# Kernel optimization log

Measured on AMD Instinct MI355X. Metric: run time of the kernel, lower is better.

The kernel has to match this reference:

```python
import jax, jax.numpy as jnp
import numpy as np

DIM = 1024
D_STATE = 16
D_CONV = 4
EXPAND = 2
D_INNER = EXPAND * DIM          # 2048
DT_RANK = DIM // 16             # 64 (ceil(1024/16))
BATCH = 4096
LN_EPS = 1e-5


def setup_inputs() -> dict:
    key = jax.random.key(0)
    ks = jax.random.split(key, 8)
    s = lambda k, shape, sc=0.02: (jax.random.normal(k, shape, jnp.float32) * sc)
    return {
        "x": jax.random.normal(ks[0], (BATCH, DIM), jnp.float32),
        "ln_gamma": jnp.ones((DIM,), jnp.float32),
        "ln_beta": jnp.zeros((DIM,), jnp.float32),
        "W_in": s(ks[1], (2 * D_INNER, DIM)),            # in_proj (no bias)
        "conv_w": s(ks[2], (D_INNER, D_CONV), 0.2),      # depthwise causal conv
        "conv_b": jnp.zeros((D_INNER,), jnp.float32),
        "W_xproj": s(ks[3], (DT_RANK + 2 * D_STATE, D_INNER)),
        "W_dt": s(ks[4], (D_INNER, DT_RANK), 0.1),
        "b_dt": s(ks[5], (D_INNER,), 0.5),
        "A_log": jnp.log(jnp.broadcast_to(
            jnp.arange(1, D_STATE + 1, dtype=jnp.float32), (D_INNER, D_STATE))),
        "Dskip": jnp.ones((D_INNER,), jnp.float32),
        "W_out": s(ks[6], (DIM, D_INNER)),               # out_proj (no bias)
    }


def _mamba_layer(x, ln_gamma, ln_beta, W_in, conv_w, conv_b,
                 W_xproj, W_dt, b_dt, A_log, Dskip, W_out):
    # x: [B, dim] -> unsqueeze(1): [B, L=1, dim]
    xs = x[:, None, :]
    # LayerNorm over last dim
    mu = jnp.mean(xs, axis=-1, keepdims=True)
    var = jnp.var(xs, axis=-1, keepdims=True)
    xn = (xs - mu) * jax.lax.rsqrt(var + LN_EPS) * ln_gamma + ln_beta
    # in_proj -> split into x, z   [B, L, d_inner] each
    xz = jnp.einsum('bld,ed->ble', xn, W_in)
    xi, z = jnp.split(xz, 2, axis=-1)
    L = xi.shape[1]
    # depthwise causal conv1d (kernel d_conv, left pad d_conv-1)
    xp = jnp.pad(xi, ((0, 0), (D_CONV - 1, 0), (0, 0)))
    xc = conv_b + sum(conv_w[:, k] * xp[:, k:k + L, :] for k in range(D_CONV))
    xc = jax.nn.silu(xc)
    # x_proj -> dt, B, C
    xdb = jnp.einsum('bld,ed->ble', xc, W_xproj)
    dt, Bm, Cm = jnp.split(xdb, [DT_RANK, DT_RANK + D_STATE], axis=-1)
    dt = jax.nn.softplus(jnp.einsum('blr,dr->bld', dt, W_dt) + b_dt)  # [B,L,d_inner]
    A = -jnp.exp(A_log)                                              # [d_inner,d_state]
    dA = jnp.exp(dt[..., None] * A)                                  # [B,L,d_inner,d_state]
    dBu = dt[..., None] * Bm[:, :, None, :] * xc[..., None]          # [B,L,d_inner,d_state]

    def step(h, inp):
        dA_l, dBu_l, C_l = inp
        h = dA_l * h + dBu_l                    # [B,d_inner,d_state]
        y = jnp.einsum('bdn,bn->bd', h, C_l)    # [B,d_inner]
        return h, y

    h0 = jnp.zeros((x.shape[0], D_INNER, D_STATE), x.dtype)
    _, ys = jax.lax.scan(step, h0, (dA.swapaxes(0, 1), dBu.swapaxes(0, 1), Cm.swapaxes(0, 1)))
    y = ys.swapaxes(0, 1) + Dskip * xc          # [B,L,d_inner]
    y = y * jax.nn.silu(z)
    out = jnp.einsum('ble,de->bld', y, W_out)   # [B,L,dim]
    return out[:, 0, :]                          # squeeze(1)


def reference(x, ln_gamma, ln_beta, W_in, conv_w, conv_b,
              W_xproj, W_dt, b_dt, A_log, Dskip, W_out):
    return _mamba_layer(x, ln_gamma, ln_beta, W_in, conv_w, conv_b,
                        W_xproj, W_dt, b_dt, A_log, Dskip, W_out)
```

## Files before the change

### kernel.cpp

```cpp
#include <hip/hip_runtime.h>
#include <hip/hip_bf16.h>
#include <stdint.h>

#define DIM     1024
#define DINNER  2048
#define BATCH   4096
#define LN_EPS  1e-5f

typedef unsigned short u16;
using f32x4  = __attribute__((ext_vector_type(4))) float;
using bf16x8 = __attribute__((ext_vector_type(8))) __bf16;

__device__ __forceinline__ float bf2f(u16 h) {
    union { unsigned u; float f; } v; v.u = ((unsigned)h) << 16; return v.f;
}
__device__ __forceinline__ u16 f2bf(float f) {
    union { float f; unsigned u; } v; v.f = f;
    unsigned r = v.u + 0x7fffu + ((v.u >> 16) & 1u);
    return (u16)(r >> 16);
}
__device__ __forceinline__ float silu_f(float x) {
    return x / (1.f + __expf(-x));
}

#define AS1 __attribute__((address_space(1)))
#define AS3 __attribute__((address_space(3)))

__device__ __forceinline__ unsigned lds_u32(const void* p) {
    return (unsigned)(unsigned long long)(const AS3 void*)p;
}

__global__ __launch_bounds__(256)
void cvt_ln(const float* __restrict__ x, const float* __restrict__ gamma,
            const float* __restrict__ beta, u16* __restrict__ xn,
            const float4* __restrict__ s0, ushort4* __restrict__ d0, int n0,
            const float4* __restrict__ s1, ushort4* __restrict__ d1, int n1,
            const float4* __restrict__ s2, ushort4* __restrict__ d2, int n2,
            const float4* __restrict__ s3, ushort4* __restrict__ d3, int n3)
{
    const int t = threadIdx.x;
    if (blockIdx.x < BATCH) {
        const int row = blockIdx.x;
        float4 v = ((const float4*)(x + (size_t)row * DIM))[t];
        float s1v = v.x + v.y + v.z + v.w;
        float s2v = v.x*v.x + v.y*v.y + v.z*v.z + v.w*v.w;
        #pragma unroll
        for (int o = 32; o > 0; o >>= 1) {
            s1v += __shfl_down(s1v, o);
            s2v += __shfl_down(s2v, o);
        }
        __shared__ float red[8];
        __shared__ float mv[2];
        const int w = t >> 6, l = t & 63;
        if (l == 0) { red[w] = s1v; red[4 + w] = s2v; }
        __syncthreads();
        if (t == 0) {
            float a = red[0] + red[1] + red[2] + red[3];
            float b = red[4] + red[5] + red[6] + red[7];
            float mu = a * (1.f / DIM);
            float var = b * (1.f / DIM) - mu * mu;
            mv[0] = mu; mv[1] = rsqrtf(var + LN_EPS);
        }
        __syncthreads();
        const float mu = mv[0], rs = mv[1];
        float4 g  = ((const float4*)gamma)[t];
        float4 be = ((const float4*)beta)[t];
        ushort4 o = make_ushort4(
            f2bf((v.x - mu) * rs * g.x + be.x),
            f2bf((v.y - mu) * rs * g.y + be.y),
            f2bf((v.z - mu) * rs * g.z + be.z),
            f2bf((v.w - mu) * rs * g.w + be.w));
        *(ushort4*)(xn + (size_t)row * DIM + t * 4) = o;
    } else {
        int i = (blockIdx.x - BATCH) * 256 + t;
        const int stride = (gridDim.x - BATCH) * 256;
        const int total = n0 + n1 + n2 + n3;
        for (; i < total; i += stride) {
            int j = i; const float4* s; ushort4* d;
            if (j < n0) { s = s0; d = d0; }
            else { j -= n0;
                if (j < n1) { s = s1; d = d1; }
                else { j -= n1;
                    if (j < n2) { s = s2; d = d2; }
                    else { j -= n2; s = s3; d = d3; }
                }
            }
            float4 v = s[j];
            d[j] = make_ushort4(f2bf(v.x), f2bf(v.y), f2bf(v.z), f2bf(v.w));
        }
    }
}

#define DSR(d, adr, OFFSTR) \
    asm volatile("ds_read_b128 %0, %1 offset:" OFFSTR : "=v"(d) : "v"(adr))
#define RD_A8(DST, A0, A1, S0, S1, S2, S3) do { \
    DSR(DST[0][0], A0, S0); DSR(DST[0][1], A1, S0); \
    DSR(DST[1][0], A0, S1); DSR(DST[1][1], A1, S1); \
    DSR(DST[2][0], A0, S2); DSR(DST[2][1], A1, S2); \
    DSR(DST[3][0], A0, S3); DSR(DST[3][1], A1, S3); } while (0)
#define RD_B4(DST, A0, A1, S0, S1) do { \
    DSR(DST[0][0], A0, S0); DSR(DST[0][1], A1, S0); \
    DSR(DST[1][0], A0, S1); DSR(DST[1][1], A1, S1); } while (0)

#define BC8(x) __builtin_bit_cast(bf16x8, x)
#define MF1(C, Av, Bv) C = __builtin_amdgcn_mfma_f32_16x16x32_bf16(BC8(Av), BC8(Bv), C, 0, 0, 0)

#define CL32_LO do { \
    _Pragma("unroll") for (int m = 0; m < 4; ++m) \
    _Pragma("unroll") for (int n = 0; n < 2; ++n) \
    _Pragma("unroll") for (int k = 0; k < 2; ++k) { \
        MF1(acc[m][n],     aLo[m][k], bC0[n][k]); \
        MF1(acc[m][n + 2], aLo[m][k], bC1[n][k]); } } while (0)
#define CL16_HI0 do { \
    _Pragma("unroll") for (int m = 0; m < 4; ++m) \
    _Pragma("unroll") for (int n = 0; n < 2; ++n) \
    _Pragma("unroll") for (int k = 0; k < 2; ++k) \
        MF1(acc[4 + m][n], aHi[m][k], bC0[n][k]); } while (0)
#define CL16_HI1 do { \
    _Pragma("unroll") for (int m = 0; m < 4; ++m) \
    _Pragma("unroll") for (int n = 0; n < 2; ++n) \
    _Pragma("unroll") for (int k = 0; k < 2; ++k) \
        MF1(acc[4 + m][n + 2], aHi[m][k], bC1[n][k]); } while (0)

#define WAIT_LGKM8 do { asm volatile("s_waitcnt lgkmcnt(8)" ::: "memory"); \
    __builtin_amdgcn_sched_barrier(0); } while (0)
#define WAIT_LGKM0 do { asm volatile("s_waitcnt lgkmcnt(0)" ::: "memory"); \
    __builtin_amdgcn_sched_barrier(0); } while (0)

#define TILE_BODY(CA0, CA1, NA0, NA1, NB0, NB1, SDA0, SDA1, SDB0, SDB1, KT) do { \
    RD_A8(aHi, CA0, CA1, "8192", "10240", "12288", "14336"); \
    WAIT_LGKM8; \
    __builtin_amdgcn_s_setprio(1); CL32_LO; __builtin_amdgcn_s_setprio(0); \
    WAIT_LGKM0; \
    asm volatile("s_waitcnt vmcnt(0)" ::: "memory"); \
    __builtin_amdgcn_s_barrier(); \
    stage(SDB0, Bb, KT); stage(SDB1, BbH, KT); \
    stage(SDA0, Ab, KT); stage(SDA1, AbH, KT); \
    __builtin_amdgcn_s_setprio(1); CL16_HI0; __builtin_amdgcn_s_setprio(0); \
    RD_B4(bC0, NB0, NB1, "0", "2048"); \
    RD_A8(aLo, NA0, NA1, "0", "2048", "4096", "6144"); \
    __builtin_amdgcn_s_setprio(1); CL16_HI1; __builtin_amdgcn_s_setprio(0); \
    RD_B4(bC1, NB0, NB1, "4096", "6144"); \
} while (0)

__global__ __launch_bounds__(512, 2)
void gemmP(const u16* __restrict__ A, const u16* __restrict__ B,
           int N, int K, int nkt,
           u16* __restrict__ dst0, u16* __restrict__ dst1,
           const float* __restrict__ conv_w, const float* __restrict__ conv_b)
{
    __shared__ __align__(16) u16 lds[2][4][8192];
    const int tid = threadIdx.x;
    const int wid = tid >> 6, l = tid & 63;
    const int wm = wid >> 2, wn = wid & 3;
    const int lr = l & 15, l16 = l >> 4;

    const int lin = blockIdx.y * 16 + blockIdx.x;
    const int xcd = lin & 7, q = lin >> 3;
    const int by = (xcd & 3) * 4 + (q >> 3);
    const int bx = (xcd >> 2) * 8 + (q & 7);
    const int brow = by * 256, bcol = bx * 256;

    const int sr = tid >> 3;
    const int skk = ((tid & 7) ^ (sr & 7)) * 8;
    const u16* Ab  = A + (size_t)(brow + sr) * K + skk;
    const u16* Bb  = B + (size_t)(bcol + sr) * K + skk;
    const u16* AbH = Ab + (size_t)128 * K;
    const u16* BbH = Bb + (size_t)128 * K;

    u16* const dA0h0 = &lds[0][0][tid * 8]; u16* const dA0h1 = &lds[0][1][tid * 8];
    u16* const dA1h0 = &lds[1][0][tid * 8]; u16* const dA1h1 = &lds[1][1][tid * 8];
    u16* const dB0h0 = &lds[0][2][tid * 8]; u16* const dB0h1 = &lds[0][3][tid * 8];
    u16* const dB1h0 = &lds[1][2][tid * 8]; u16* const dB1h1 = &lds[1][3][tid * 8];

    const unsigned cxb0 = (unsigned)(((0 + l16) ^ (l & 7)) * 16);
    const unsigned cxb1 = (unsigned)(((4 + l16) ^ (l & 7)) * 16);
    const unsigned aB0 = lds_u32(&lds[0][wm][0]) + (unsigned)(lr * 128);
    const unsigned bB0 = lds_u32(&lds[0][2 + (wn >> 1)][0]) + (unsigned)((wn & 1) * 8192 + lr * 128);
    const unsigned adA00 = aB0 + cxb0, adA01 = aB0 + cxb1;
    const unsigned adA10 = adA00 + 65536, adA11 = adA01 + 65536;
    const unsigned adB00 = bB0 + cxb0, adB01 = bB0 + cxb1;
    const unsigned adB10 = adB00 + 65536, adB11 = adB01 + 65536;

    f32x4 acc[8][4] = {};
    float4 aLo[4][2], aHi[4][2], bC0[2][2], bC1[2][2];

    auto stage = [&](u16* dst, const u16* srcrow, int kt) {
        const u16* s = srcrow + (size_t)kt * 64;
        __builtin_amdgcn_global_load_lds((const AS1 void*)s, (AS3 void*)dst, 16, 0, 0);
        __builtin_amdgcn_global_load_lds((const AS1 void*)(s + (size_t)64 * K),
                                         (AS3 void*)(dst + 4096), 16, 0, 0);
    };

    stage(dB0h0, Bb, 0);  stage(dB0h1, BbH, 0);
    stage(dA0h0, Ab, 0);  stage(dA0h1, AbH, 0);
    stage(dB1h0, Bb, 1);  stage(dB1h1, BbH, 1);
    stage(dA1h0, Ab, 1);  stage(dA1h1, AbH, 1);
    asm volatile("s_waitcnt vmcnt(8)" ::: "memory");
    __builtin_amdgcn_s_barrier();
    RD_B4(bC0, adB00, adB01, "0", "2048");
    RD_B4(bC1, adB00, adB01, "4096", "6144");
    RD_A8(aLo, adA00, adA01, "0", "2048", "4096", "6144");

    const int niter = nkt >> 1;
    for (int i = 0; i < niter; ++i) {
        const int T = 2 * i;
        const int k2 = (T + 2 < nkt) ? T + 2 : nkt - 1;
        const int k3 = (T + 3 < nkt) ? T + 3 : nkt - 1;
        TILE_BODY(adA00, adA01, adA10, adA11, adB10, adB11,
                  dA0h0, dA0h1, dB0h0, dB0h1, k2);
        TILE_BODY(adA10, adA11, adA00, adA01, adB00, adB01,
                  dA1h0, dA1h1, dB1h0, dB1h1, k3);
    }

    asm volatile("s_waitcnt vmcnt(0) lgkmcnt(0)" ::: "memory");
    __builtin_amdgcn_s_barrier();

    float cb[4], cw[4];
    const bool isxc = (bcol < DINNER);
    if (isxc) {
        #pragma unroll
        for (int n = 0; n < 4; ++n) {
            const int cg = bcol + wn * 64 + n * 16 + lr;
            cb[n] = conv_b[cg]; cw[n] = conv_w[cg * 4 + 3];
        }
    }
    u16* eb = &lds[0][0][0];
    #pragma unroll
    for (int m = 0; m < 8; ++m)
        #pragma unroll
        for (int n = 0; n < 4; ++n)
            #pragma unroll
            for (int r = 0; r < 4; ++r) {
                const int rl = wm * 128 + m * 16 + l16 * 4 + r;
                const int cl = wn * 64 + n * 16 + lr;
                float v = acc[m][n][r];
                v = isxc ? silu_f(cb[n] + cw[n] * v) : silu_f(v);
                eb[rl * 256 + (cl ^ ((rl & 15) << 4))] = f2bf(v);
            }
    __syncthreads();

    u16* base = isxc ? (dst0 + bcol) : (dst1 + (bcol - DINNER));
    #pragma unroll
    for (int it = 0; it < 16; ++it) {
        const int idx = it * 4096 + tid * 8;
        const int r = idx >> 8, c = idx & 255;
        uint4 v = *(const uint4*)(eb + r * 256 + ((c ^ ((r & 15) << 4))));
        *(uint4*)(base + (size_t)(brow + r) * DINNER + c) = v;
    }
}

__global__ __launch_bounds__(256)
void gemm_xproj(const u16* __restrict__ xcb, const u16* __restrict__ Wx,
                float* __restrict__ P)
{
    __shared__ __align__(16) u16 Xs[64 * 64];
    __shared__ __align__(16) u16 Ws[96 * 64];
    const int t = threadIdx.x, w = t >> 6, l = t & 63;
    const int brow = blockIdx.x * 64;
    const int ks = blockIdx.y;
    const int lr = l & 15, l16 = l >> 4;
    const int skk = ((l & 7) ^ (l >> 3)) * 8;
    const u16* Xbase = xcb + (size_t)(brow + (l >> 3)) * DINNER + skk;
    const u16* Wbase = Wx + (size_t)(l >> 3) * DINNER + skk;

    f32x4 acc[6] = {};
    const int kend = ks * 512 + 512;
    for (int k0 = ks * 512; k0 < kend; k0 += 64) {
        #pragma unroll
        for (int c = 0; c < 2; ++c) {
            const int seg = c * 4 + w;
            __builtin_amdgcn_global_load_lds(
                (const AS1 void*)(Xbase + (size_t)seg * 8 * DINNER + k0),
                (AS3 void*)(&Xs[seg * 512]), 16, 0, 0);
        }
        #pragma unroll
        for (int c = 0; c < 3; ++c) {
            const int seg = c * 4 + w;
            __builtin_amdgcn_global_load_lds(
                (const AS1 void*)(Wbase + (size_t)seg * 8 * DINNER + k0),
                (AS3 void*)(&Ws[seg * 512]), 16, 0, 0);
        }
        __syncthreads();
        #pragma unroll
        for (int kk = 0; kk < 2; ++kk) {
            const int ra = w * 16 + lr;
            bf16x8 av = *(const bf16x8*)(&Xs[ra * 64 + (((kk * 4 + l16) ^ (ra & 7)) * 8)]);
            #pragma unroll
            for (int n = 0; n < 6; ++n) {
                const int rb = n * 16 + lr;
                bf16x8 bv = *(const bf16x8*)(&Ws[rb * 64 + (((kk * 4 + l16) ^ (rb & 7)) * 8)]);
                acc[n] = __builtin_amdgcn_mfma_f32_16x16x32_bf16(av, bv, acc[n], 0, 0, 0);
            }
        }
        __syncthreads();
    }
    #pragma unroll
    for (int n = 0; n < 6; ++n)
        #pragma unroll
        for (int r = 0; r < 4; ++r) {
            const int row = brow + w * 16 + l16 * 4 + r;
            const int col = n * 16 + lr;
            P[((size_t)ks * 96 + col) * BATCH + row] = acc[n][r];
        }
}

__global__ __launch_bounds__(256)
void finish_xdb(const float* __restrict__ P, u16* __restrict__ dtb, float* __restrict__ sbuf)
{
    const int b = blockIdx.x * 256 + threadIdx.x;
    #pragma unroll 8
    for (int c = 0; c < 64; ++c) {
        float v = P[((size_t)0 * 96 + c) * BATCH + b] + P[((size_t)1 * 96 + c) * BATCH + b]
                + P[((size_t)2 * 96 + c) * BATCH + b] + P[((size_t)3 * 96 + c) * BATCH + b];
        dtb[(size_t)b * 64 + c] = f2bf(v);
    }
    float s = 0.f;
    for (int n = 0; n < 16; ++n) {
        float Bv = 0.f, Cv = 0.f;
        #pragma unroll
        for (int ks = 0; ks < 4; ++ks) {
            Bv += P[((size_t)ks * 96 + 64 + n) * BATCH + b];
            Cv += P[((size_t)ks * 96 + 80 + n) * BATCH + b];
        }
        s += Bv * Cv;
    }
    sbuf[b] = s;
}

__global__ __launch_bounds__(256)
void gemm_dt_y(const u16* __restrict__ dtb, const u16* __restrict__ Wdt,
               const float* __restrict__ b_dt, const float* __restrict__ Dskip,
               const float* __restrict__ s,
               const u16* __restrict__ xcb, const u16* __restrict__ szb,
               u16* __restrict__ y)
{
    __shared__ __align__(16) u16 Ds[64 * 64];
    __shared__ __align__(16) u16 Ws[128 * 64];
    __shared__ __align__(16) u16 dts[64 * 128];
    const int t = threadIdx.x, w = t >> 6, l = t & 63;
    const int wr = w >> 1, wc = w & 1;
    const int brow = blockIdx.y * 64;
    const int bcol = blockIdx.x * 128;
    const int lr = l & 15, l16 = l >> 4;
    const int skk = ((l & 7) ^ (l >> 3)) * 8;

    {
        const u16* Dbase = dtb + (size_t)(brow + (l >> 3)) * 64 + skk;
        const u16* Wbase = Wdt + (size_t)(bcol + (l >> 3)) * 64 + skk;
        #pragma unroll
        for (int c = 0; c < 2; ++c) {
            const int seg = c * 4 + w;
            __builtin_amdgcn_global_load_lds(
                (const AS1 void*)(Dbase + (size_t)seg * 8 * 64),
                (AS3 void*)(&Ds[seg * 512]), 16, 0, 0);
        }
        #pragma unroll
        for (int c = 0; c < 4; ++c) {
            const int seg = c * 4 + w;
            __builtin_amdgcn_global_load_lds(
                (const AS1 void*)(Wbase + (size_t)seg * 8 * 64),
                (AS3 void*)(&Ws[seg * 512]), 16, 0, 0);
        }
    }
    __syncthreads();

    f32x4 acc[2][4] = {};
    #pragma unroll
    for (int kk = 0; kk < 2; ++kk) {
        bf16x8 av[2], bv[4];
        #pragma unroll
        for (int m = 0; m < 2; ++m) {
            const int r = wr * 32 + m * 16 + lr;
            av[m] = *(const bf16x8*)(&Ds[r * 64 + (((kk * 4 + l16) ^ (r & 7)) * 8)]);
        }
        #pragma unroll
        for (int n = 0; n < 4; ++n) {
            const int r = wc * 64 + n * 16 + lr;
            bv[n] = *(const bf16x8*)(&Ws[r * 64 + (((kk * 4 + l16) ^ (r & 7)) * 8)]);
        }
        #pragma unroll
        for (int m = 0; m < 2; ++m)
            #pragma unroll
            for (int n = 0; n < 4; ++n)
                acc[m][n] = __builtin_amdgcn_mfma_f32_16x16x32_bf16(av[m], bv[n], acc[m][n], 0, 0, 0);
    }

    #pragma unroll
    for (int m = 0; m < 2; ++m)
        #pragma unroll
        for (int n = 0; n < 4; ++n)
            #pragma unroll
            for (int r = 0; r < 4; ++r) {
                const int row = wr * 32 + m * 16 + l16 * 4 + r;
                const int col = wc * 64 + n * 16 + lr;
                float v = acc[m][n][r] + b_dt[bcol + col];
                float dt = (v > 20.f) ? v : log1pf(__expf(v));
                dts[row * 128 + (col ^ ((row & 7) << 4))] = f2bf(dt);
            }
    __syncthreads();

    const int rlo = t >> 4;
    const int cg  = (t & 15) * 8;
    #pragma unroll
    for (int rr = 0; rr < 4; ++rr) {
        const int row = rr * 16 + rlo;
        const int grow = brow + row;
        const float sr = s[grow];
        uint4 dv = *(const uint4*)(&dts[row * 128 + ((cg ^ ((row & 7) << 4)))]);
        uint4 xv = *(const uint4*)(xcb + (size_t)grow * DINNER + bcol + cg);
        uint4 zv = *(const uint4*)(szb + (size_t)grow * DINNER + bcol + cg);
        float4 D0 = *(const float4*)(Dskip + bcol + cg);
        float4 D1 = *(const float4*)(Dskip + bcol + cg + 4);
        const float* Dp = &D0.x;
        uint4 ov;
        unsigned* op = (unsigned*)&ov;
        #pragma unroll
        for (int k = 0; k < 4; ++k) {
            unsigned du = ((const unsigned*)&dv)[k];
            unsigned xu = ((const unsigned*)&xv)[k];
            unsigned zu = ((const unsigned*)&zv)[k];
            float Da = (k < 2) ? Dp[2 * k]     : (&D1.x)[2 * (k - 2)];
            float Db = (k < 2) ? Dp[2 * k + 1] : (&D1.x)[2 * (k - 2) + 1];
            float y0 = (bf2f((u16)du) * sr + Da) * bf2f((u16)xu) * bf2f((u16)zu);
            float y1 = (bf2f((u16)(du >> 16)) * sr + Db) * bf2f((u16)(xu >> 16)) * bf2f((u16)(zu >> 16));
            op[k] = (unsigned)f2bf(y0) | ((unsigned)f2bf(y1) << 16);
        }
        *(uint4*)(y + (size_t)grow * DINNER + bcol + cg) = ov;
    }
}

__global__ __launch_bounds__(256, 2)
void gemm4n(const u16* __restrict__ A, const u16* __restrict__ Bm,
            float* __restrict__ out)
{
    __shared__ __align__(16) u16 lds[2][12288];
    const int t = threadIdx.x, w = t >> 6, l = t & 63;
    const int wr = w >> 1, wc = w & 1;
    const int lr = l & 15, l16 = l >> 4;

    const int lin = blockIdx.y * 8 + blockIdx.x;
    const int xcd = lin & 7, q = lin >> 3;
    const int by = xcd * 8 + (q >> 3);
    const int bx = q & 7;
    const int brow = by * 64, bcol = bx * 128;
    const int K = DINNER, nkt = 32;

    auto stage = [&](int buf, int kt) {
        #pragma unroll
        for (int c = 0; c < 2; ++c) {
            const int o = c * 256 + t;
            const int sr = o >> 3;
            const int sc = (o & 7) ^ (sr & 7);
            __builtin_amdgcn_global_load_lds(
                (const AS1 void*)(A + (size_t)(brow + sr) * K + kt * 64 + sc * 8),
                (AS3 void*)(&lds[buf][o * 8]), 16, 0, 0);
        }
        #pragma unroll
        for (int c = 0; c < 4; ++c) {
            const int o = c * 256 + t;
            const int sr = o >> 3;
            const int sc = (o & 7) ^ (sr & 7);
            __builtin_amdgcn_global_load_lds(
                (const AS1 void*)(Bm + (size_t)(bcol + sr) * K + kt * 64 + sc * 8),
                (AS3 void*)(&lds[buf][4096 + o * 8]), 16, 0, 0);
        }
    };

    f32x4 acc[2][4] = {};

    stage(0, 0);
    stage(1, 1);
    asm volatile("s_waitcnt vmcnt(6)" ::: "memory");
    __builtin_amdgcn_s_barrier();

    for (int kt = 0; kt < nkt; ++kt) {
        const int cur = kt & 1;
        #pragma unroll
        for (int kk = 0; kk < 2; ++kk) {
            bf16x8 af[2], bf[4];
            #pragma unroll
            for (int m = 0; m < 2; ++m) {
                const int r = wr * 32 + m * 16 + lr;
                af[m] = *(const bf16x8*)(&lds[cur][r * 64 + (((kk * 4 + l16) ^ (r & 7)) * 8)]);
            }
            #pragma unroll
            for (int n = 0; n < 4; ++n) {
                const int r = wc * 64 + n * 16 + lr;
                bf[n] = *(const bf16x8*)(&lds[cur][4096 + r * 64 + (((kk * 4 + l16) ^ (r & 7)) * 8)]);
            }
            #pragma unroll
            for (int m = 0; m < 2; ++m)
                #pragma unroll
                for (int n = 0; n < 4; ++n)
                    acc[m][n] = __builtin_amdgcn_mfma_f32_16x16x32_bf16(af[m], bf[n], acc[m][n], 0, 0, 0);
        }
        __builtin_amdgcn_sched_barrier(0);
        __builtin_amdgcn_s_barrier();
        const int t2 = (kt + 2 < nkt) ? kt + 2 : nkt - 1;
        stage(cur, t2);
        asm volatile("s_waitcnt vmcnt(6)" ::: "memory");
        __builtin_amdgcn_sched_barrier(0);
        __builtin_amdgcn_s_barrier();
    }

    asm volatile("s_waitcnt vmcnt(0) lgkmcnt(0)" ::: "memory");
    __builtin_amdgcn_s_barrier();

    float* eb = (float*)&lds[0][0];
    #pragma unroll
    for (int m = 0; m < 2; ++m)
        #pragma unroll
        for (int n = 0; n < 4; ++n)
            #pragma unroll
            for (int r = 0; r < 4; ++r) {
                const int row = wr * 32 + m * 16 + l16 * 4 + r;
                const int col = wc * 64 + n * 16 + lr;
                eb[row * 128 + (col ^ ((row & 7) << 2))] = acc[m][n][r];
            }
    __syncthreads();
    #pragma unroll
    for (int it = 0; it < 8; ++it) {
        const int idx = it * 1024 + t * 4;
        const int row = idx >> 7, col = idx & 127;
        float4 v = *(const float4*)(eb + row * 128 + ((col ^ ((row & 7) << 2))));
        *(float4*)(out + (size_t)(brow + row) * DIM + bcol + col) = v;
    }
}

extern "C" void kernel_launch(void* const* d_in, const int* in_sizes, int n_in,
                              void* d_out, int out_size, void* d_ws, size_t ws_size,
                              hipStream_t stream) {
    const float* x      = (const float*)d_in[0];
    const float* ln_g   = (const float*)d_in[1];
    const float* ln_b   = (const float*)d_in[2];
    const float* W_in   = (const float*)d_in[3];
    const float* conv_w = (const float*)d_in[4];
    const float* conv_b = (const float*)d_in[5];
    const float* W_xp   = (const float*)d_in[6];
    const float* W_dt   = (const float*)d_in[7];
    const float* b_dt   = (const float*)d_in[8];
    const float* Dskip  = (const float*)d_in[10];
    const float* W_out  = (const float*)d_in[11];
    float* out = (float*)d_out;

    char* ws = (char*)d_ws;
    const size_t MB = 1u << 20;
    u16*  W_in_b  = (u16*)(ws);
    u16*  xn      = (u16*)(ws + 8 * MB);
    u16*  xcb     = (u16*)(ws + 16 * MB);
    u16*  szb     = (u16*)(ws + 32 * MB);
    float* Pxp    = (float*)(ws + 48 * MB);
    u16*  W_xp_b  = (u16*)(ws + 55 * MB);
    u16*  W_dt_b  = (u16*)(ws + 56 * MB);
    u16*  dtb     = (u16*)(ws + 57 * MB);
    float* sbuf   = (float*)(ws + 58 * MB);
    u16*  W_out_b = (u16*)(ws + 64 * MB);
    u16*  yb      = (u16*)(ws + 68 * MB);

    cvt_ln<<<BATCH + 2048, 256, 0, stream>>>(
        x, ln_g, ln_b, xn,
        (const float4*)W_in,  (ushort4*)W_in_b,  (2 * DINNER * DIM) / 4,
        (const float4*)W_out, (ushort4*)W_out_b, (DIM * DINNER) / 4,
        (const float4*)W_xp,  (ushort4*)W_xp_b,  (96 * DINNER) / 4,
        (const float4*)W_dt,  (ushort4*)W_dt_b,  (DINNER * 64) / 4);

    gemmP<<<dim3(4096 / 256, BATCH / 256, 1), 512, 0, stream>>>(
        xn, W_in_b, 4096, DIM, DIM / 64, xcb, szb, conv_w, conv_b);

    gemm_xproj<<<dim3(BATCH / 64, 4), 256, 0, stream>>>(xcb, W_xp_b, Pxp);

    finish_xdb<<<BATCH / 256, 256, 0, stream>>>(Pxp, dtb, sbuf);

    gemm_dt_y<<<dim3(DINNER / 128, BATCH / 64), 256, 0, stream>>>(
        dtb, W_dt_b, b_dt, Dskip, sbuf, xcb, szb, yb);

    gemm4n<<<dim3(DIM / 128, BATCH / 64), 256, 0, stream>>>(yb, W_out_b, out);
}
```

Measured before the change: 146.0 us.

## Replace hand-scheduled 256x256 in_proj GEMM with simpler 64x128 tiled kernel

Swaps the large 256x256-tile, 512-thread in_proj GEMM, with inline-asm LDS reads, priority hints and XCD-aware block remapping, for a plain 64x128-tile, 256-thread double-buffered kernel. The aim is more blocks in flight (2048 instead of 256) for better CU coverage and lower scheduling complexity. In exchange each block reuses far less data, so global and LDS traffic per FLOP goes up, and the hand-tuned software pipelining is lost.

```diff
diff --git a/kernel.cpp b/kernel.cpp
--- a/kernel.cpp
+++ b/kernel.cpp
@@ -25,10 +25,6 @@
 
 #define AS1 __attribute__((address_space(1)))
 #define AS3 __attribute__((address_space(3)))
-
-__device__ __forceinline__ unsigned lds_u32(const void* p) {
-    return (unsigned)(unsigned long long)(const AS3 void*)p;
-}
 
 __global__ __launch_bounds__(256)
 void cvt_ln(const float* __restrict__ x, const float* __restrict__ gamma,
@@ -91,161 +87,109 @@
     }
 }
 
-#define DSR(d, adr, OFFSTR) \
-    asm volatile("ds_read_b128 %0, %1 offset:" OFFSTR : "=v"(d) : "v"(adr))
-#define RD_A8(DST, A0, A1, S0, S1, S2, S3) do { \
-    DSR(DST[0][0], A0, S0); DSR(DST[0][1], A1, S0); \
-    DSR(DST[1][0], A0, S1); DSR(DST[1][1], A1, S1); \
-    DSR(DST[2][0], A0, S2); DSR(DST[2][1], A1, S2); \
-    DSR(DST[3][0], A0, S3); DSR(DST[3][1], A1, S3); } while (0)
-#define RD_B4(DST, A0, A1, S0, S1) do { \
-    DSR(DST[0][0], A0, S0); DSR(DST[0][1], A1, S0); \
-    DSR(DST[1][0], A0, S1); DSR(DST[1][1], A1, S1); } while (0)
-
-#define BC8(x) __builtin_bit_cast(bf16x8, x)
-#define MF1(C, Av, Bv) C = __builtin_amdgcn_mfma_f32_16x16x32_bf16(BC8(Av), BC8(Bv), C, 0, 0, 0)
-
-#define CL32_LO do { \
-    _Pragma("unroll") for (int m = 0; m < 4; ++m) \
-    _Pragma("unroll") for (int n = 0; n < 2; ++n) \
-    _Pragma("unroll") for (int k = 0; k < 2; ++k) { \
-        MF1(acc[m][n],     aLo[m][k], bC0[n][k]); \
-        MF1(acc[m][n + 2], aLo[m][k], bC1[n][k]); } } while (0)
-#define CL16_HI0 do { \
-    _Pragma("unroll") for (int m = 0; m < 4; ++m) \
-    _Pragma("unroll") for (int n = 0; n < 2; ++n) \
-    _Pragma("unroll") for (int k = 0; k < 2; ++k) \
-        MF1(acc[4 + m][n], aHi[m][k], bC0[n][k]); } while (0)
-#define CL16_HI1 do { \
-    _Pragma("unroll") for (int m = 0; m < 4; ++m) \
-    _Pragma("unroll") for (int n = 0; n < 2; ++n) \
-    _Pragma("unroll") for (int k = 0; k < 2; ++k) \
-        MF1(acc[4 + m][n + 2], aHi[m][k], bC1[n][k]); } while (0)
-
-#define WAIT_LGKM8 do { asm volatile("s_waitcnt lgkmcnt(8)" ::: "memory"); \
-    __builtin_amdgcn_sched_barrier(0); } while (0)
-#define WAIT_LGKM0 do { asm volatile("s_waitcnt lgkmcnt(0)" ::: "memory"); \
-    __builtin_amdgcn_sched_barrier(0); } while (0)
-
-#define TILE_BODY(CA0, CA1, NA0, NA1, NB0, NB1, SDA0, SDA1, SDB0, SDB1, KT) do { \
-    RD_A8(aHi, CA0, CA1, "8192", "10240", "12288", "14336"); \
-    WAIT_LGKM8; \
-    __builtin_amdgcn_s_setprio(1); CL32_LO; __builtin_amdgcn_s_setprio(0); \
-    WAIT_LGKM0; \
-    asm volatile("s_waitcnt vmcnt(0)" ::: "memory"); \
-    __builtin_amdgcn_s_barrier(); \
-    stage(SDB0, Bb, KT); stage(SDB1, BbH, KT); \
-    stage(SDA0, Ab, KT); stage(SDA1, AbH, KT); \
-    __builtin_amdgcn_s_setprio(1); CL16_HI0; __builtin_amdgcn_s_setprio(0); \
-    RD_B4(bC0, NB0, NB1, "0", "2048"); \
-    RD_A8(aLo, NA0, NA1, "0", "2048", "4096", "6144"); \
-    __builtin_amdgcn_s_setprio(1); CL16_HI1; __builtin_amdgcn_s_setprio(0); \
-    RD_B4(bC1, NB0, NB1, "4096", "6144"); \
-} while (0)
-
-__global__ __launch_bounds__(512, 2)
-void gemmP(const u16* __restrict__ A, const u16* __restrict__ B,
-           int N, int K, int nkt,
-           u16* __restrict__ dst0, u16* __restrict__ dst1,
-           const float* __restrict__ conv_w, const float* __restrict__ conv_b)
+__global__ __launch_bounds__(256, 2)
+void gemm1n(const u16* __restrict__ A, const u16* __restrict__ Bm,
+            u16* __restrict__ xc, u16* __restrict__ sz,
+            const float* __restrict__ conv_w, const float* __restrict__ conv_b)
 {
-    __shared__ __align__(16) u16 lds[2][4][8192];
-    const int tid = threadIdx.x;
-    const int wid = tid >> 6, l = tid & 63;
-    const int wm = wid >> 2, wn = wid & 3;
+    __shared__ __align__(16) u16 lds[2][12288];
+    const int t = threadIdx.x, w = t >> 6, l = t & 63;
+    const int wr = w >> 1, wc = w & 1;
     const int lr = l & 15, l16 = l >> 4;
-
-    const int lin = blockIdx.y * 16 + blockIdx.x;
-    const int xcd = lin & 7, q = lin >> 3;
-    const int by = (xcd & 3) * 4 + (q >> 3);
-    const int bx = (xcd >> 2) * 8 + (q & 7);
-    const int brow = by * 256, bcol = bx * 256;
-
-    const int sr = tid >> 3;
-    const int skk = ((tid & 7) ^ (sr & 7)) * 8;
-    const u16* Ab  = A + (size_t)(brow + sr) * K + skk;
-    const u16* Bb  = B + (size_t)(bcol + sr) * K + skk;
-    const u16* AbH = Ab + (size_t)128 * K;
-    const u16* BbH = Bb + (size_t)128 * K;
-
-    u16* const dA0h0 = &lds[0][0][tid * 8]; u16* const dA0h1 = &lds[0][1][tid * 8];
-    u16* const dA1h0 = &lds[1][0][tid * 8]; u16* const dA1h1 = &lds[1][1][tid * 8];
-    u16* const dB0h0 = &lds[0][2][tid * 8]; u16* const dB0h1 = &lds[0][3][tid * 8];
-    u16* const dB1h0 = &lds[1][2][tid * 8]; u16* const dB1h1 = &lds[1][3][tid * 8];
-
-    const unsigned cxb0 = (unsigned)(((0 + l16) ^ (l & 7)) * 16);
-    const unsigned cxb1 = (unsigned)(((4 + l16) ^ (l & 7)) * 16);
-    const unsigned aB0 = lds_u32(&lds[0][wm][0]) + (unsigned)(lr * 128);
-    const unsigned bB0 = lds_u32(&lds[0][2 + (wn >> 1)][0]) + (unsigned)((wn & 1) * 8192 + lr * 128);
-    const unsigned adA00 = aB0 + cxb0, adA01 = aB0 + cxb1;
-    const unsigned adA10 = adA00 + 65536, adA11 = adA01 + 65536;
-    const unsigned adB00 = bB0 + cxb0, adB01 = bB0 + cxb1;
-    const unsigned adB10 = adB00 + 65536, adB11 = adB01 + 65536;
-
-    f32x4 acc[8][4] = {};
-    float4 aLo[4][2], aHi[4][2], bC0[2][2], bC1[2][2];
-
-    auto stage = [&](u16* dst, const u16* srcrow, int kt) {
-        const u16* s = srcrow + (size_t)kt * 64;
-        __builtin_amdgcn_global_load_lds((const AS1 void*)s, (AS3 void*)dst, 16, 0, 0);
-        __builtin_amdgcn_global_load_lds((const AS1 void*)(s + (size_t)64 * K),
-                                         (AS3 void*)(dst + 4096), 16, 0, 0);
+    const int brow = blockIdx.y * 64, bcol = blockIdx.x * 128;
+    const int K = DIM, nkt = 16;
+
+    auto stage = [&](int buf, int kt) {
+        #pragma unroll
+        for (int c = 0; c < 2; ++c) {
+            const int o = c * 256 + t;
+            const int sr = o >> 3;
+            const int sc = (o & 7) ^ (sr & 7);
+            __builtin_amdgcn_global_load_lds(
+                (const AS1 void*)(A + (size_t)(brow + sr) * K + kt * 64 + sc * 8),
+                (AS3 void*)(&lds[buf][o * 8]), 16, 0, 0);
+        }
+        #pragma unroll
+        for (int c = 0; c < 4; ++c) {
+            const int o = c * 256 + t;
+            const int sr = o >> 3;
+            const int sc = (o & 7) ^ (sr & 7);
+            __builtin_amdgcn_global_load_lds(
+                (const AS1 void*)(Bm + (size_t)(bcol + sr) * K + kt * 64 + sc * 8),
+                (AS3 void*)(&lds[buf][4096 + o * 8]), 16, 0, 0);
+        }
     };
 
-    stage(dB0h0, Bb, 0);  stage(dB0h1, BbH, 0);
-    stage(dA0h0, Ab, 0);  stage(dA0h1, AbH, 0);
-    stage(dB1h0, Bb, 1);  stage(dB1h1, BbH, 1);
-    stage(dA1h0, Ab, 1);  stage(dA1h1, AbH, 1);
-    asm volatile("s_waitcnt vmcnt(8)" ::: "memory");
+    f32x4 acc[2][4] = {};
+
+    stage(0, 0);
+    stage(1, 1);
+    asm volatile("s_waitcnt vmcnt(6)" ::: "memory");
     __builtin_amdgcn_s_barrier();
-    RD_B4(bC0, adB00, adB01, "0", "2048");
-    RD_B4(bC1, adB00, adB01, "4096", "6144");
-    RD_A8(aLo, adA00, adA01, "0", "2048", "4096", "6144");
-
-    const int niter = nkt >> 1;
-    for (int i = 0; i < niter; ++i) {
-        const int T = 2 * i;
-        const int k2 = (T + 2 < nkt) ? T + 2 : nkt - 1;
-        const int k3 = (T + 3 < nkt) ? T + 3 : nkt - 1;
-        TILE_BODY(adA00, adA01, adA10, adA11, adB10, adB11,
-                  dA0h0, dA0h1, dB0h0, dB0h1, k2);
-        TILE_BODY(adA10, adA11, adA00, adA01, adB00, adB01,
-                  dA1h0, dA1h1, dB1h0, dB1h1, k3);
+
+    for (int kt = 0; kt < nkt; ++kt) {
+        const int cur = kt & 1;
+        #pragma unroll
+        for (int kk = 0; kk < 2; ++kk) {
+            bf16x8 af[2], bf[4];
+            #pragma unroll
+            for (int m = 0; m < 2; ++m) {
+                const int r = wr * 32 + m * 16 + lr;
+                af[m] = *(const bf16x8*)(&lds[cur][r * 64 + (((kk * 4 + l16) ^ (r & 7)) * 8)]);
+            }
+            #pragma unroll
+            for (int n = 0; n < 4; ++n) {
+                const int r = wc * 64 + n * 16 + lr;
+                bf[n] = *(const bf16x8*)(&lds[cur][4096 + r * 64 + (((kk * 4 + l16) ^ (r & 7)) * 8)]);
+            }
+            #pragma unroll
+            for (int m = 0; m < 2; ++m)
+                #pragma unroll
+                for (int n = 0; n < 4; ++n)
+                    acc[m][n] = __builtin_amdgcn_mfma_f32_16x16x32_bf16(af[m], bf[n], acc[m][n], 0, 0, 0);
+        }
+        __builtin_amdgcn_sched_barrier(0);
+        __builtin_amdgcn_s_barrier();
+        const int t2 = (kt + 2 < nkt) ? kt + 2 : nkt - 1;
+        stage(cur, t2);
+        asm volatile("s_waitcnt vmcnt(6)" ::: "memory");
+        __builtin_amdgcn_sched_barrier(0);
+        __builtin_amdgcn_s_barrier();
     }
 
     asm volatile("s_waitcnt vmcnt(0) lgkmcnt(0)" ::: "memory");
     __builtin_amdgcn_s_barrier();
 
+    const bool isxc = (bcol < DINNER);
     float cb[4], cw[4];
-    const bool isxc = (bcol < DINNER);
     if (isxc) {
         #pragma unroll
         for (int n = 0; n < 4; ++n) {
-            const int cg = bcol + wn * 64 + n * 16 + lr;
+            const int cg = bcol + wc * 64 + n * 16 + lr;
             cb[n] = conv_b[cg]; cw[n] = conv_w[cg * 4 + 3];
         }
     }
-    u16* eb = &lds[0][0][0];
-    #pragma unroll
-    for (int m = 0; m < 8; ++m)
+    u16* eb = &lds[0][0];
+    #pragma unroll
+    for (int m = 0; m < 2; ++m)
         #pragma unroll
         for (int n = 0; n < 4; ++n)
             #pragma unroll
             for (int r = 0; r < 4; ++r) {
-                const int rl = wm * 128 + m * 16 + l16 * 4 + r;
-                const int cl = wn * 64 + n * 16 + lr;
+                const int row = wr * 32 + m * 16 + l16 * 4 + r;
+                const int col = wc * 64 + n * 16 + lr;
                 float v = acc[m][n][r];
                 v = isxc ? silu_f(cb[n] + cw[n] * v) : silu_f(v);
-                eb[rl * 256 + (cl ^ ((rl & 15) << 4))] = f2bf(v);
+                eb[row * 128 + (col ^ ((row & 7) << 3))] = f2bf(v);
             }
     __syncthreads();
 
-    u16* base = isxc ? (dst0 + bcol) : (dst1 + (bcol - DINNER));
-    #pragma unroll
-    for (int it = 0; it < 16; ++it) {
-        const int idx = it * 4096 + tid * 8;
-        const int r = idx >> 8, c = idx & 255;
-        uint4 v = *(const uint4*)(eb + r * 256 + ((c ^ ((r & 15) << 4))));
+    u16* base = isxc ? (xc + bcol) : (sz + (bcol - DINNER));
+    #pragma unroll
+    for (int it = 0; it < 4; ++it) {
+        const int idx = it * 2048 + t * 8;
+        const int r = idx >> 7, c = idx & 127;
+        uint4 v = *(const uint4*)(eb + r * 128 + ((c ^ ((r & 7) << 3))));
         *(uint4*)(base + (size_t)(brow + r) * DINNER + c) = v;
     }
 }
@@ -565,8 +509,8 @@
         (const float4*)W_xp,  (ushort4*)W_xp_b,  (96 * DINNER) / 4,
         (const float4*)W_dt,  (ushort4*)W_dt_b,  (DINNER * 64) / 4);
 
-    gemmP<<<dim3(4096 / 256, BATCH / 256, 1), 512, 0, stream>>>(
-        xn, W_in_b, 4096, DIM, DIM / 64, xcb, szb, conv_w, conv_b);
+    gemm1n<<<dim3(4096 / 128, BATCH / 64), 256, 0, stream>>>(
+        xn, W_in_b, xcb, szb, conv_w, conv_b);
 
     gemm_xproj<<<dim3(BATCH / 64, 4), 256, 0, stream>>>(xcb, W_xp_b, Pxp);
 
```

After: 154.6 us. +5.9%, slower.

## Split xproj finish kernel across more blocks, drop XCD remap, change epilogue swizzle

Applied to the files above, without the earlier changes.

The finish kernel was launched with only 16 blocks. It is now split into a 16x6 grid: four blocks per column group reduce dt slices, and two handle halves of the B·C dot product, writing two partial sums that gemm_dt_y adds. The in_proj GEMM also drops its XCD-aware block remapping in favour of plain blockIdx tiling. Its epilogue LDS swizzle changes from (row&15) to ((row>>2)&3), which may change LDS bank conflicts. Dropping the remap risks worse L2 locality across XCDs.

```diff
diff --git a/kernel.cpp b/kernel.cpp
--- a/kernel.cpp
+++ b/kernel.cpp
@@ -154,12 +154,7 @@
     const int wid = tid >> 6, l = tid & 63;
     const int wm = wid >> 2, wn = wid & 3;
     const int lr = l & 15, l16 = l >> 4;
-
-    const int lin = blockIdx.y * 16 + blockIdx.x;
-    const int xcd = lin & 7, q = lin >> 3;
-    const int by = (xcd & 3) * 4 + (q >> 3);
-    const int bx = (xcd >> 2) * 8 + (q & 7);
-    const int brow = by * 256, bcol = bx * 256;
+    const int brow = blockIdx.y * 256, bcol = blockIdx.x * 256;
 
     const int sr = tid >> 3;
     const int skk = ((tid & 7) ^ (sr & 7)) * 8;
@@ -236,7 +231,7 @@
                 const int cl = wn * 64 + n * 16 + lr;
                 float v = acc[m][n][r];
                 v = isxc ? silu_f(cb[n] + cw[n] * v) : silu_f(v);
-                eb[rl * 256 + (cl ^ ((rl & 15) << 4))] = f2bf(v);
+                eb[rl * 256 + (cl ^ (((rl >> 2) & 3) << 4))] = f2bf(v);
             }
     __syncthreads();
 
@@ -245,7 +240,7 @@
     for (int it = 0; it < 16; ++it) {
         const int idx = it * 4096 + tid * 8;
         const int r = idx >> 8, c = idx & 255;
-        uint4 v = *(const uint4*)(eb + r * 256 + ((c ^ ((r & 15) << 4))));
+        uint4 v = *(const uint4*)(eb + r * 256 + (c ^ (((r >> 2) & 3) << 4)));
         *(uint4*)(base + (size_t)(brow + r) * DINNER + c) = v;
     }
 }
@@ -306,32 +301,40 @@
 }
 
 __global__ __launch_bounds__(256)
-void finish_xdb(const float* __restrict__ P, u16* __restrict__ dtb, float* __restrict__ sbuf)
+void finish_split(const float* __restrict__ P, u16* __restrict__ dtb,
+                  float* __restrict__ s0, float* __restrict__ s1)
 {
     const int b = blockIdx.x * 256 + threadIdx.x;
-    #pragma unroll 8
-    for (int c = 0; c < 64; ++c) {
-        float v = P[((size_t)0 * 96 + c) * BATCH + b] + P[((size_t)1 * 96 + c) * BATCH + b]
-                + P[((size_t)2 * 96 + c) * BATCH + b] + P[((size_t)3 * 96 + c) * BATCH + b];
-        dtb[(size_t)b * 64 + c] = f2bf(v);
-    }
-    float s = 0.f;
-    for (int n = 0; n < 16; ++n) {
-        float Bv = 0.f, Cv = 0.f;
-        #pragma unroll
-        for (int ks = 0; ks < 4; ++ks) {
-            Bv += P[((size_t)ks * 96 + 64 + n) * BATCH + b];
-            Cv += P[((size_t)ks * 96 + 80 + n) * BATCH + b];
-        }
-        s += Bv * Cv;
-    }
-    sbuf[b] = s;
+    const int y = blockIdx.y;
+    if (y < 4) {
+        #pragma unroll
+        for (int j = 0; j < 16; ++j) {
+            const int c = y * 16 + j;
+            float v = P[((size_t)0 * 96 + c) * BATCH + b] + P[((size_t)1 * 96 + c) * BATCH + b]
+                    + P[((size_t)2 * 96 + c) * BATCH + b] + P[((size_t)3 * 96 + c) * BATCH + b];
+            dtb[(size_t)b * 64 + c] = f2bf(v);
+        }
+    } else {
+        const int n0 = (y == 4) ? 0 : 8;
+        float s = 0.f;
+        #pragma unroll
+        for (int n = 0; n < 8; ++n) {
+            float Bv = 0.f, Cv = 0.f;
+            #pragma unroll
+            for (int ks = 0; ks < 4; ++ks) {
+                Bv += P[((size_t)ks * 96 + 64 + n0 + n) * BATCH + b];
+                Cv += P[((size_t)ks * 96 + 80 + n0 + n) * BATCH + b];
+            }
+            s += Bv * Cv;
+        }
+        ((y == 4) ? s0 : s1)[b] = s;
+    }
 }
 
 __global__ __launch_bounds__(256)
 void gemm_dt_y(const u16* __restrict__ dtb, const u16* __restrict__ Wdt,
                const float* __restrict__ b_dt, const float* __restrict__ Dskip,
-               const float* __restrict__ s,
+               const float* __restrict__ s0, const float* __restrict__ s1,
                const u16* __restrict__ xcb, const u16* __restrict__ szb,
                u16* __restrict__ y)
 {
@@ -406,7 +409,7 @@
     for (int rr = 0; rr < 4; ++rr) {
         const int row = rr * 16 + rlo;
         const int grow = brow + row;
-        const float sr = s[grow];
+        const float sr = s0[grow] + s1[grow];
         uint4 dv = *(const uint4*)(&dts[row * 128 + ((cg ^ ((row & 7) << 4)))]);
         uint4 xv = *(const uint4*)(xcb + (size_t)grow * DINNER + bcol + cg);
         uint4 zv = *(const uint4*)(szb + (size_t)grow * DINNER + bcol + cg);
@@ -554,7 +557,8 @@
     u16*  W_xp_b  = (u16*)(ws + 55 * MB);
     u16*  W_dt_b  = (u16*)(ws + 56 * MB);
     u16*  dtb     = (u16*)(ws + 57 * MB);
-    float* sbuf   = (float*)(ws + 58 * MB);
+    float* sbuf0  = (float*)(ws + 58 * MB);
+    float* sbuf1  = (float*)(ws + 59 * MB);
     u16*  W_out_b = (u16*)(ws + 64 * MB);
     u16*  yb      = (u16*)(ws + 68 * MB);
 
@@ -570,10 +574,10 @@
 
     gemm_xproj<<<dim3(BATCH / 64, 4), 256, 0, stream>>>(xcb, W_xp_b, Pxp);
 
-    finish_xdb<<<BATCH / 256, 256, 0, stream>>>(Pxp, dtb, sbuf);
+    finish_split<<<dim3(16, 6), 256, 0, stream>>>(Pxp, dtb, sbuf0, sbuf1);
 
     gemm_dt_y<<<dim3(DINNER / 128, BATCH / 64), 256, 0, stream>>>(
-        dtb, W_dt_b, b_dt, Dskip, sbuf, xcb, szb, yb);
+        dtb, W_dt_b, b_dt, Dskip, sbuf0, sbuf1, xcb, szb, yb);
 
     gemm4n<<<dim3(DIM / 128, BATCH / 64), 256, 0, stream>>>(yb, W_out_b, out);
 }
```

Result: faster. 124.1 us (-15.0%).

## Fuse x_proj split-K GEMM with its reduction and simplify gemmP tile mapping

Applied to the files above, without the earlier changes.

Replaces the split-K x_proj GEMM plus a separate finish kernel with a single kernel where each block handles 16 rows. Its four waves each take a K quarter with double-buffered async LDS loads, then reduce through LDS and write dt and the B·C dot product directly. This removes the fp32 partial buffer round trip through global memory and one kernel launch. It also drops the XCD-aware block remapping in gemmP in favour of plain blockIdx mapping and changes the epilogue LDS swizzle. That could change L2 locality and LDS bank-conflict behaviour.

```diff
diff --git a/kernel.cpp b/kernel.cpp
--- a/kernel.cpp
+++ b/kernel.cpp
@@ -154,12 +154,7 @@
     const int wid = tid >> 6, l = tid & 63;
     const int wm = wid >> 2, wn = wid & 3;
     const int lr = l & 15, l16 = l >> 4;
-
-    const int lin = blockIdx.y * 16 + blockIdx.x;
-    const int xcd = lin & 7, q = lin >> 3;
-    const int by = (xcd & 3) * 4 + (q >> 3);
-    const int bx = (xcd >> 2) * 8 + (q & 7);
-    const int brow = by * 256, bcol = bx * 256;
+    const int brow = blockIdx.y * 256, bcol = blockIdx.x * 256;
 
     const int sr = tid >> 3;
     const int skk = ((tid & 7) ^ (sr & 7)) * 8;
@@ -236,7 +231,7 @@
                 const int cl = wn * 64 + n * 16 + lr;
                 float v = acc[m][n][r];
                 v = isxc ? silu_f(cb[n] + cw[n] * v) : silu_f(v);
-                eb[rl * 256 + (cl ^ ((rl & 15) << 4))] = f2bf(v);
+                eb[rl * 256 + (cl ^ (((rl >> 2) & 3) << 4))] = f2bf(v);
             }
     __syncthreads();
 
@@ -245,93 +240,103 @@
     for (int it = 0; it < 16; ++it) {
         const int idx = it * 4096 + tid * 8;
         const int r = idx >> 8, c = idx & 255;
-        uint4 v = *(const uint4*)(eb + r * 256 + ((c ^ ((r & 15) << 4))));
+        uint4 v = *(const uint4*)(eb + r * 256 + (c ^ (((r >> 2) & 3) << 4)));
         *(uint4*)(base + (size_t)(brow + r) * DINNER + c) = v;
     }
 }
 
 __global__ __launch_bounds__(256)
-void gemm_xproj(const u16* __restrict__ xcb, const u16* __restrict__ Wx,
-                float* __restrict__ P)
+void gemm_xdb(const u16* __restrict__ xcb, const u16* __restrict__ Wx,
+              u16* __restrict__ dtb, float* __restrict__ sbuf)
 {
-    __shared__ __align__(16) u16 Xs[64 * 64];
-    __shared__ __align__(16) u16 Ws[96 * 64];
+    __shared__ __align__(16) u16 slc[4][2][7168];
     const int t = threadIdx.x, w = t >> 6, l = t & 63;
-    const int brow = blockIdx.x * 64;
-    const int ks = blockIdx.y;
     const int lr = l & 15, l16 = l >> 4;
-    const int skk = ((l & 7) ^ (l >> 3)) * 8;
-    const u16* Xbase = xcb + (size_t)(brow + (l >> 3)) * DINNER + skk;
-    const u16* Wbase = Wx + (size_t)(l >> 3) * DINNER + skk;
+    const int brow = blockIdx.x * 16;
+    const int wk = w * 512;
+
+    auto stageX = [&](u16* dst, int step) {
+        #pragma unroll
+        for (int i = 0; i < 2; ++i) {
+            const int o = i * 512 + l * 8;
+            const int row = o >> 6;
+            const int c8 = ((o >> 3) & 7) ^ (row & 7);
+            __builtin_amdgcn_global_load_lds(
+                (const AS1 void*)(xcb + (size_t)(brow + row) * DINNER + wk + step * 64 + c8 * 8),
+                (AS3 void*)(dst + o), 16, 0, 0);
+        }
+    };
+    auto stageW = [&](u16* dst, int step) {
+        #pragma unroll
+        for (int i = 0; i < 12; ++i) {
+            const int o = i * 512 + l * 8;
+            const int row = o >> 6;
+            const int c8 = ((o >> 3) & 7) ^ (row & 7);
+            __builtin_amdgcn_global_load_lds(
+                (const AS1 void*)(Wx + (size_t)row * DINNER + wk + step * 64 + c8 * 8),
+                (AS3 void*)(dst + 1024 + o), 16, 0, 0);
+        }
+    };
 
     f32x4 acc[6] = {};
-    const int kend = ks * 512 + 512;
-    for (int k0 = ks * 512; k0 < kend; k0 += 64) {
-        #pragma unroll
-        for (int c = 0; c < 2; ++c) {
-            const int seg = c * 4 + w;
-            __builtin_amdgcn_global_load_lds(
-                (const AS1 void*)(Xbase + (size_t)seg * 8 * DINNER + k0),
-                (AS3 void*)(&Xs[seg * 512]), 16, 0, 0);
-        }
-        #pragma unroll
-        for (int c = 0; c < 3; ++c) {
-            const int seg = c * 4 + w;
-            __builtin_amdgcn_global_load_lds(
-                (const AS1 void*)(Wbase + (size_t)seg * 8 * DINNER + k0),
-                (AS3 void*)(&Ws[seg * 512]), 16, 0, 0);
-        }
-        __syncthreads();
+
+    stageX(&slc[w][0][0], 0); stageW(&slc[w][0][0], 0);
+    stageX(&slc[w][1][0], 1); stageW(&slc[w][1][0], 1);
+    asm volatile("s_waitcnt vmcnt(14)" ::: "memory");
+    __builtin_amdgcn_sched_barrier(0);
+
+    for (int s = 0; s < 8; ++s) {
+        const u16* sl = &slc[w][s & 1][0];
         #pragma unroll
         for (int kk = 0; kk < 2; ++kk) {
-            const int ra = w * 16 + lr;
-            bf16x8 av = *(const bf16x8*)(&Xs[ra * 64 + (((kk * 4 + l16) ^ (ra & 7)) * 8)]);
+            bf16x8 av = *(const bf16x8*)(sl + lr * 64 + (((kk * 4 + l16) ^ (lr & 7)) * 8));
             #pragma unroll
             for (int n = 0; n < 6; ++n) {
                 const int rb = n * 16 + lr;
-                bf16x8 bv = *(const bf16x8*)(&Ws[rb * 64 + (((kk * 4 + l16) ^ (rb & 7)) * 8)]);
+                bf16x8 bv = *(const bf16x8*)(sl + 1024 + rb * 64 + (((kk * 4 + l16) ^ (rb & 7)) * 8));
                 acc[n] = __builtin_amdgcn_mfma_f32_16x16x32_bf16(av, bv, acc[n], 0, 0, 0);
             }
         }
-        __syncthreads();
-    }
+        __builtin_amdgcn_sched_barrier(0);
+        const int s2 = (s + 2 < 8) ? s + 2 : 7;
+        u16* dst = &slc[w][s & 1][0];
+        stageX(dst, s2); stageW(dst, s2);
+        asm volatile("s_waitcnt vmcnt(14)" ::: "memory");
+        __builtin_amdgcn_sched_barrier(0);
+    }
+
+    asm volatile("s_waitcnt vmcnt(0)" ::: "memory");
+    __syncthreads();
+
+    float* red = (float*)&slc[0][0][0];
     #pragma unroll
     for (int n = 0; n < 6; ++n)
         #pragma unroll
-        for (int r = 0; r < 4; ++r) {
-            const int row = brow + w * 16 + l16 * 4 + r;
-            const int col = n * 16 + lr;
-            P[((size_t)ks * 96 + col) * BATCH + row] = acc[n][r];
-        }
-}
-
-__global__ __launch_bounds__(256)
-void finish_xdb(const float* __restrict__ P, u16* __restrict__ dtb, float* __restrict__ sbuf)
-{
-    const int b = blockIdx.x * 256 + threadIdx.x;
-    #pragma unroll 8
-    for (int c = 0; c < 64; ++c) {
-        float v = P[((size_t)0 * 96 + c) * BATCH + b] + P[((size_t)1 * 96 + c) * BATCH + b]
-                + P[((size_t)2 * 96 + c) * BATCH + b] + P[((size_t)3 * 96 + c) * BATCH + b];
-        dtb[(size_t)b * 64 + c] = f2bf(v);
-    }
-    float s = 0.f;
-    for (int n = 0; n < 16; ++n) {
-        float Bv = 0.f, Cv = 0.f;
-        #pragma unroll
-        for (int ks = 0; ks < 4; ++ks) {
-            Bv += P[((size_t)ks * 96 + 64 + n) * BATCH + b];
-            Cv += P[((size_t)ks * 96 + 80 + n) * BATCH + b];
-        }
-        s += Bv * Cv;
-    }
-    sbuf[b] = s;
+        for (int r = 0; r < 4; ++r)
+            red[w * 1536 + (l16 * 4 + r) * 96 + n * 16 + lr] = acc[n][r];
+    __syncthreads();
+    #pragma unroll
+    for (int i = 0; i < 6; ++i) {
+        const int idx = i * 256 + t;
+        float v = red[idx] + red[1536 + idx] + red[3072 + idx] + red[4608 + idx];
+        red[idx] = v;
+        const int row = idx / 96, col = idx - row * 96;
+        if (col < 64) dtb[(size_t)(brow + row) * 64 + col] = f2bf(v);
+    }
+    __syncthreads();
+    if (t < 16) {
+        float s = 0.f;
+        #pragma unroll
+        for (int n = 0; n < 16; ++n)
+            s += red[t * 96 + 64 + n] * red[t * 96 + 80 + n];
+        sbuf[brow + t] = s;
+    }
 }
 
 __global__ __launch_bounds__(256)
 void gemm_dt_y(const u16* __restrict__ dtb, const u16* __restrict__ Wdt,
                const float* __restrict__ b_dt, const float* __restrict__ Dskip,
-               const float* __restrict__ s,
+               const float* __restrict__ sbuf,
                const u16* __restrict__ xcb, const u16* __restrict__ szb,
                u16* __restrict__ y)
 {
@@ -406,7 +411,7 @@
     for (int rr = 0; rr < 4; ++rr) {
         const int row = rr * 16 + rlo;
         const int grow = brow + row;
-        const float sr = s[grow];
+        const float sr = sbuf[grow];
         uint4 dv = *(const uint4*)(&dts[row * 128 + ((cg ^ ((row & 7) << 4)))]);
         uint4 xv = *(const uint4*)(xcb + (size_t)grow * DINNER + bcol + cg);
         uint4 zv = *(const uint4*)(szb + (size_t)grow * DINNER + bcol + cg);
@@ -550,7 +555,6 @@
     u16*  xn      = (u16*)(ws + 8 * MB);
     u16*  xcb     = (u16*)(ws + 16 * MB);
     u16*  szb     = (u16*)(ws + 32 * MB);
-    float* Pxp    = (float*)(ws + 48 * MB);
     u16*  W_xp_b  = (u16*)(ws + 55 * MB);
     u16*  W_dt_b  = (u16*)(ws + 56 * MB);
     u16*  dtb     = (u16*)(ws + 57 * MB);
@@ -568,9 +572,7 @@
     gemmP<<<dim3(4096 / 256, BATCH / 256, 1), 512, 0, stream>>>(
         xn, W_in_b, 4096, DIM, DIM / 64, xcb, szb, conv_w, conv_b);
 
-    gemm_xproj<<<dim3(BATCH / 64, 4), 256, 0, stream>>>(xcb, W_xp_b, Pxp);
-
-    finish_xdb<<<BATCH / 256, 256, 0, stream>>>(Pxp, dtb, sbuf);
+    gemm_xdb<<<BATCH / 16, 256, 0, stream>>>(xcb, W_xp_b, dtb, sbuf);
 
     gemm_dt_y<<<dim3(DINNER / 128, BATCH / 64), 256, 0, stream>>>(
         dtb, W_dt_b, b_dt, Dskip, sbuf, xcb, szb, yb);
```

Measured after the change: 119.4 us (median of 2 runs). -18.2%, faster.
